# Optimization experiments

Measured on AMD Instinct MI355X. Metric: run time of the kernel, lower is better.

Reference implementation:

```python
import jax, jax.numpy as jnp
import numpy as np

N_NODES = 50000
N_EDGES = 800000
IN_C, HID_C, OUT_C = 100, 128, 40


def setup_inputs() -> dict:
    key = jax.random.key(0)
    ks = jax.random.split(key, 10)
    x = jax.random.normal(ks[0], (N_NODES, IN_C), dtype=jnp.float32)
    edge_index = jax.random.randint(ks[1], (2, N_EDGES), 0, N_NODES, dtype=jnp.int64)

    def lin(k, fan_in, fan_out):
        kw, kb = jax.random.split(k)
        bound = 1.0 / np.sqrt(fan_in)
        W = jax.random.uniform(kw, (fan_in, fan_out), minval=-bound, maxval=bound, dtype=jnp.float32)
        b = jax.random.uniform(kb, (fan_out,), minval=-bound, maxval=bound, dtype=jnp.float32)
        return W, b

    W1a, b1a = lin(ks[2], IN_C, HID_C)
    W1b, b1b = lin(ks[3], HID_C, HID_C)
    W2a, b2a = lin(ks[4], HID_C, OUT_C)
    W2b, b2b = lin(ks[5], OUT_C, OUT_C)
    return {"x": x, "edge_index": edge_index,
            "W1a": W1a, "b1a": b1a, "W1b": W1b, "b1b": b1b,
            "W2a": W2a, "b2a": b2a, "W2b": W2b, "b2b": b2b}


def _gin_aggregate(x, src, dst):
    # GINConv with eps=0: (1+eps)*x_i + sum_{j in N(i)} x_j
    msg_sum = jax.ops.segment_sum(x[src], dst, num_segments=N_NODES)
    return x + msg_sum


def reference(x, edge_index, W1a, b1a, W1b, b1b, W2a, b2a, W2b, b2b):
    src, dst = edge_index[0], edge_index[1]
    # ---- layer 1: GINConv(MLP[in, hid, hid]) + ReLU (dropout is identity in eval)
    h = _gin_aggregate(x, src, dst)                      # [N, in]
    h = jax.nn.relu(h @ W1a + b1a) @ W1b + b1b           # [N, hid]
    h = jax.nn.relu(h)
    # ---- layer 2: GINConv(MLP[hid, out, out]), no trailing act
    h = _gin_aggregate(h, src, dst)                      # [N, hid]
    logits = jax.nn.relu(h @ W2a + b2a) @ W2b + b2b      # [N, out]
    return jax.nn.log_softmax(logits, axis=1)
```

## Files before the change

kernel.cpp:

```cpp
#include <hip/hip_runtime.h>

#define NNODES 50000
#define INC 100
#define HIDC 128
#define OUTC 40
#define NB2 200
#define BSZ2 250
#define CAP2 6400
#define BIN_BLOCKS 256
#define EPB 13

typedef short bf16x8 __attribute__((ext_vector_type(8)));
typedef float f32x4 __attribute__((ext_vector_type(4)));

__device__ __forceinline__ unsigned short f2bf(float f) {
    unsigned int u = __float_as_uint(f);
    unsigned int r = (u + 0x7FFFu + ((u >> 16) & 1u)) >> 16;
    return (unsigned short)r;
}
__device__ __forceinline__ unsigned int pack2(float a, float b) {
    return (unsigned int)f2bf(a) | ((unsigned int)f2bf(b) << 16);
}
__device__ __forceinline__ float4 bf4(uint2 a) {
    return make_float4(__uint_as_float(a.x << 16), __uint_as_float(a.x & 0xFFFF0000u),
                       __uint_as_float(a.y << 16), __uint_as_float(a.y & 0xFFFF0000u));
}

__global__ __launch_bounds__(256) void prep_all(const float2* __restrict__ x2,
                                                unsigned int* __restrict__ xh, int n2,
                                                const float* __restrict__ W1a,
                                                unsigned short* __restrict__ Wt1a,
                                                const float* __restrict__ W1b,
                                                unsigned short* __restrict__ Wt1b,
                                                const float* __restrict__ W2a,
                                                unsigned short* __restrict__ Wt2a,
                                                const float* __restrict__ W2b,
                                                unsigned short* __restrict__ Wt2b,
                                                int* __restrict__ bcnt) {
    if (blockIdx.x == 0 && threadIdx.x < NB2) bcnt[threadIdx.x] = 0;
    int i = blockIdx.x * 256 + threadIdx.x;
    if (i < n2) {
        float2 v = x2[i];
        xh[i] = pack2(v.x, v.y);
        return;
    }
    i -= n2;
    if (i < 128 * 128) {
        int j = i >> 7, k = i & 127;
        Wt1a[i] = f2bf((k < INC) ? W1a[k * HIDC + j] : 0.f);
        return;
    }
    i -= 128 * 128;
    if (i < 128 * 128) {
        int j = i >> 7, k = i & 127;
        Wt1b[i] = f2bf(W1b[k * HIDC + j]);
        return;
    }
    i -= 128 * 128;
    if (i < 48 * 128) {
        int j = i >> 7, k = i & 127;
        Wt2a[i] = f2bf((j < OUTC) ? W2a[k * OUTC + j] : 0.f);
        return;
    }
    i -= 48 * 128;
    if (i < 48 * 64) {
        int j = i >> 6, k = i & 63;
        Wt2b[i] = f2bf((j < OUTC && k < OUTC) ? W2b[k * OUTC + j] : 0.f);
        return;
    }
}

__global__ __launch_bounds__(256) void bin_pairs(const int* __restrict__ src,
                                                 const int* __restrict__ dst,
                                                 int* __restrict__ bcnt,
                                                 unsigned int* __restrict__ pairs, int E) {
    __shared__ int bcount[NB2];
    __shared__ int bbase[NB2];
    __shared__ int bpos[NB2];
    int t = threadIdx.x;
    if (t < NB2) bcount[t] = 0;
    __syncthreads();
    int lo = (int)((long long)E * blockIdx.x / BIN_BLOCKS);
    int hi = (int)((long long)E * (blockIdx.x + 1) / BIN_BLOCKS);
    int myd[EPB];
#pragma unroll
    for (int k = 0; k < EPB; ++k) {
        int e = lo + t + k * 256;
        int d = (e < hi) ? dst[e] : -1;
        myd[k] = d;
        if (d >= 0) atomicAdd(&bcount[d / BSZ2], 1);
    }
    __syncthreads();
    if (t < NB2) {
        bbase[t] = atomicAdd(&bcnt[t], bcount[t]);
        bpos[t] = 0;
    }
    __syncthreads();
#pragma unroll
    for (int k = 0; k < EPB; ++k) {
        int d = myd[k];
        if (d >= 0) {
            int e = lo + t + k * 256;
            int s = src[e];
            int b = d / BSZ2;
            int rk = atomicAdd(&bpos[b], 1);
            pairs[(size_t)b * CAP2 + bbase[b] + rk] =
                ((unsigned int)d << 16) | (unsigned int)s;
        }
    }
}

__global__ __launch_bounds__(256) void build_bucket(const unsigned int* __restrict__ pairs,
                                                    const int* __restrict__ bcnt,
                                                    int* __restrict__ offs,
                                                    unsigned short* __restrict__ csr) {
    __shared__ int hist[BSZ2];
    __shared__ int cur[BSZ2];
    __shared__ int wsum[4];
    __shared__ int redbuf[4];
    __shared__ unsigned short lcsr[CAP2];
    __shared__ int base_s;

    const int b = blockIdx.x;
    const int t = threadIdx.x;
    const int lane = t & 63, wv = t >> 6;

    {
        int v = (t < b) ? bcnt[t] : 0;
#pragma unroll
        for (int off = 32; off; off >>= 1) v += __shfl_xor(v, off);
        if (lane == 0) redbuf[wv] = v;
    }
    if (t < BSZ2) hist[t] = 0;
    __syncthreads();
    if (t == 0) base_s = redbuf[0] + redbuf[1] + redbuf[2] + redbuf[3];

    const int cnt = bcnt[b];
    const unsigned int* P = pairs + (size_t)b * CAP2;
    const int nlo = b * BSZ2;
    __syncthreads();

    for (int i = t; i < cnt; i += 256)
        atomicAdd(&hist[(int)(P[i] >> 16) - nlo], 1);
    __syncthreads();

    {
        int v = (t < BSZ2) ? hist[t] : 0;
        int incl = v;
#pragma unroll
        for (int off = 1; off < 64; off <<= 1) {
            int u = __shfl_up(incl, off);
            if (lane >= off) incl += u;
        }
        if (lane == 63) wsum[wv] = incl;
        __syncthreads();
        int wbase = 0;
#pragma unroll
        for (int j = 0; j < 4; ++j)
            if (j < wv) wbase += wsum[j];
        int excl = wbase + incl - v;
        if (t < BSZ2) {
            cur[t] = excl;
            offs[nlo + t] = base_s + excl;
        }
        if (b == NB2 - 1 && t == 0) offs[NNODES] = base_s + cnt;
    }
    __syncthreads();

    for (int i = t; i < cnt; i += 256) {
        unsigned int pr = P[i];
        int pos = atomicAdd(&cur[(int)(pr >> 16) - nlo], 1);
        lcsr[pos] = (unsigned short)(pr & 0xFFFFu);
    }
    __syncthreads();

    for (int i = t; i < cnt; i += 256) csr[base_s + i] = lcsr[i];
}

__global__ __launch_bounds__(256) void agg_wide_bf(const float4* __restrict__ self,
                                                   const uint2* __restrict__ featbf,
                                                   const int* __restrict__ offs,
                                                   const unsigned short* __restrict__ csr,
                                                   unsigned short* __restrict__ Abf, int N) {
    constexpr int C4 = 25;
    int node = blockIdx.x * 8 + (threadIdx.x >> 5);
    int l = threadIdx.x & 31;
    if (node >= N) return;
    if (l >= C4) {
        *reinterpret_cast<uint2*>(&Abf[(size_t)node * 128 + l * 4]) = make_uint2(0u, 0u);
        return;
    }
    int s = offs[node], e = offs[node + 1];
    float4 acc = self[(size_t)node * C4 + l];
    int i = s;
    for (; i + 16 <= e; i += 16) {
        int n0 = (int)csr[i + 0],  n1 = (int)csr[i + 1];
        int n2 = (int)csr[i + 2],  n3 = (int)csr[i + 3];
        int n4 = (int)csr[i + 4],  n5 = (int)csr[i + 5];
        int n6 = (int)csr[i + 6],  n7 = (int)csr[i + 7];
        int n8 = (int)csr[i + 8],  n9 = (int)csr[i + 9];
        int na = (int)csr[i + 10], nb = (int)csr[i + 11];
        int nc = (int)csr[i + 12], nd = (int)csr[i + 13];
        int ne = (int)csr[i + 14], nf = (int)csr[i + 15];
        float4 v0 = bf4(featbf[(size_t)n0 * C4 + l]);
        float4 v1 = bf4(featbf[(size_t)n1 * C4 + l]);
        float4 v2 = bf4(featbf[(size_t)n2 * C4 + l]);
        float4 v3 = bf4(featbf[(size_t)n3 * C4 + l]);
        float4 v4 = bf4(featbf[(size_t)n4 * C4 + l]);
        float4 v5 = bf4(featbf[(size_t)n5 * C4 + l]);
        float4 v6 = bf4(featbf[(size_t)n6 * C4 + l]);
        float4 v7 = bf4(featbf[(size_t)n7 * C4 + l]);
        float4 v8 = bf4(featbf[(size_t)n8 * C4 + l]);
        float4 v9 = bf4(featbf[(size_t)n9 * C4 + l]);
        float4 va = bf4(featbf[(size_t)na * C4 + l]);
        float4 vb = bf4(featbf[(size_t)nb * C4 + l]);
        float4 vc = bf4(featbf[(size_t)nc * C4 + l]);
        float4 vd = bf4(featbf[(size_t)nd * C4 + l]);
        float4 ve = bf4(featbf[(size_t)ne * C4 + l]);
        float4 vf = bf4(featbf[(size_t)nf * C4 + l]);
        acc.x += (((v0.x + v1.x) + (v2.x + v3.x)) + ((v4.x + v5.x) + (v6.x + v7.x))) +
                 (((v8.x + v9.x) + (va.x + vb.x)) + ((vc.x + vd.x) + (ve.x + vf.x)));
        acc.y += (((v0.y + v1.y) + (v2.y + v3.y)) + ((v4.y + v5.y) + (v6.y + v7.y))) +
                 (((v8.y + v9.y) + (va.y + vb.y)) + ((vc.y + vd.y) + (ve.y + vf.y)));
        acc.z += (((v0.z + v1.z) + (v2.z + v3.z)) + ((v4.z + v5.z) + (v6.z + v7.z))) +
                 (((v8.z + v9.z) + (va.z + vb.z)) + ((vc.z + vd.z) + (ve.z + vf.z)));
        acc.w += (((v0.w + v1.w) + (v2.w + v3.w)) + ((v4.w + v5.w) + (v6.w + v7.w))) +
                 (((v8.w + v9.w) + (va.w + vb.w)) + ((vc.w + vd.w) + (ve.w + vf.w)));
    }
    for (; i + 8 <= e; i += 8) {
        int n0 = (int)csr[i + 0], n1 = (int)csr[i + 1];
        int n2 = (int)csr[i + 2], n3 = (int)csr[i + 3];
        int n4 = (int)csr[i + 4], n5 = (int)csr[i + 5];
        int n6 = (int)csr[i + 6], n7 = (int)csr[i + 7];
        float4 v0 = bf4(featbf[(size_t)n0 * C4 + l]);
        float4 v1 = bf4(featbf[(size_t)n1 * C4 + l]);
        float4 v2 = bf4(featbf[(size_t)n2 * C4 + l]);
        float4 v3 = bf4(featbf[(size_t)n3 * C4 + l]);
        float4 v4 = bf4(featbf[(size_t)n4 * C4 + l]);
        float4 v5 = bf4(featbf[(size_t)n5 * C4 + l]);
        float4 v6 = bf4(featbf[(size_t)n6 * C4 + l]);
        float4 v7 = bf4(featbf[(size_t)n7 * C4 + l]);
        acc.x += ((v0.x + v1.x) + (v2.x + v3.x)) + ((v4.x + v5.x) + (v6.x + v7.x));
        acc.y += ((v0.y + v1.y) + (v2.y + v3.y)) + ((v4.y + v5.y) + (v6.y + v7.y));
        acc.z += ((v0.z + v1.z) + (v2.z + v3.z)) + ((v4.z + v5.z) + (v6.z + v7.z));
        acc.w += ((v0.w + v1.w) + (v2.w + v3.w)) + ((v4.w + v5.w) + (v6.w + v7.w));
    }
    for (; i + 4 <= e; i += 4) {
        int n0 = (int)csr[i + 0], n1 = (int)csr[i + 1];
        int n2 = (int)csr[i + 2], n3 = (int)csr[i + 3];
        float4 v0 = bf4(featbf[(size_t)n0 * C4 + l]);
        float4 v1 = bf4(featbf[(size_t)n1 * C4 + l]);
        float4 v2 = bf4(featbf[(size_t)n2 * C4 + l]);
        float4 v3 = bf4(featbf[(size_t)n3 * C4 + l]);
        acc.x += (v0.x + v1.x) + (v2.x + v3.x);
        acc.y += (v0.y + v1.y) + (v2.y + v3.y);
        acc.z += (v0.z + v1.z) + (v2.z + v3.z);
        acc.w += (v0.w + v1.w) + (v2.w + v3.w);
    }
    for (; i < e; ++i) {
        int sn = (int)csr[i];
        float4 v = bf4(featbf[(size_t)sn * C4 + l]);
        acc.x += v.x; acc.y += v.y; acc.z += v.z; acc.w += v.w;
    }
    *reinterpret_cast<uint2*>(&Abf[(size_t)node * 128 + l * 4]) =
        make_uint2(pack2(acc.x, acc.y), pack2(acc.z, acc.w));
}

__global__ __launch_bounds__(256) void fused_mlp(const unsigned short* __restrict__ Abf,
                                                 const unsigned short* __restrict__ Wt1a,
                                                 const float* __restrict__ b1a,
                                                 const unsigned short* __restrict__ Wt1b,
                                                 const float* __restrict__ b1b,
                                                 const unsigned short* __restrict__ Wt2a,
                                                 unsigned short* __restrict__ Tb, int N) {
    constexpr int LDW = 136;
    __shared__ unsigned short As[64 * LDW];
    __shared__ unsigned short Ws[128 * LDW];
    __shared__ float bs1[128], bs2[128];

    const int tid = threadIdx.x;
    const int n0 = blockIdx.x * 64;

#pragma unroll
    for (int i = 0; i < 4; ++i) {
        int idx = tid + i * 256;
        int row = idx >> 4, c = idx & 15;
        int n = n0 + row;
        uint4 v = make_uint4(0u, 0u, 0u, 0u);
        if (n < N) v = *reinterpret_cast<const uint4*>(&Abf[(size_t)n * 128 + c * 8]);
        *reinterpret_cast<uint4*>(&As[row * LDW + c * 8]) = v;
    }
#pragma unroll
    for (int i = 0; i < 8; ++i) {
        int idx = tid + i * 256;
        int row = idx >> 4, c = idx & 15;
        *reinterpret_cast<uint4*>(&Ws[row * LDW + c * 8]) =
            *reinterpret_cast<const uint4*>(&Wt1a[(size_t)row * 128 + c * 8]);
    }
    if (tid < 128) { bs1[tid] = b1a[tid]; bs2[tid] = b1b[tid]; }
    __syncthreads();

    const int w = tid >> 6, l = tid & 63;
    const int wr = w >> 1, wc = w & 1;
    const int r = l & 15, g = l >> 4;

    f32x4 acc[2][4];
#pragma unroll
    for (int rt = 0; rt < 2; ++rt)
#pragma unroll
        for (int ct = 0; ct < 4; ++ct) {
            float b = bs1[wc * 64 + ct * 16 + r];
            acc[rt][ct] = (f32x4){b, b, b, b};
        }
#pragma unroll
    for (int s = 0; s < 4; ++s) {
        bf16x8 af[2], bfr[4];
#pragma unroll
        for (int rt = 0; rt < 2; ++rt)
            af[rt] = *reinterpret_cast<const bf16x8*>(
                &As[(wr * 32 + rt * 16 + r) * LDW + s * 32 + g * 8]);
#pragma unroll
        for (int ct = 0; ct < 4; ++ct)
            bfr[ct] = *reinterpret_cast<const bf16x8*>(
                &Ws[(wc * 64 + ct * 16 + r) * LDW + s * 32 + g * 8]);
#pragma unroll
        for (int rt = 0; rt < 2; ++rt)
#pragma unroll
            for (int ct = 0; ct < 4; ++ct)
                acc[rt][ct] = __builtin_amdgcn_mfma_f32_16x16x32_bf16(
                    af[rt], bfr[ct], acc[rt][ct], 0, 0, 0);
    }
    __syncthreads();

#pragma unroll
    for (int rt = 0; rt < 2; ++rt)
#pragma unroll
        for (int reg = 0; reg < 4; ++reg) {
            int row = wr * 32 + rt * 16 + 4 * g + reg;
#pragma unroll
            for (int ct = 0; ct < 4; ++ct) {
                int col = wc * 64 + ct * 16 + r;
                As[row * LDW + col] = f2bf(fmaxf(acc[rt][ct][reg], 0.f));
            }
        }
#pragma unroll
    for (int i = 0; i < 8; ++i) {
        int idx = tid + i * 256;
        int row = idx >> 4, c = idx & 15;
        *reinterpret_cast<uint4*>(&Ws[row * LDW + c * 8]) =
            *reinterpret_cast<const uint4*>(&Wt1b[(size_t)row * 128 + c * 8]);
    }
    __syncthreads();

#pragma unroll
    for (int rt = 0; rt < 2; ++rt)
#pragma unroll
        for (int ct = 0; ct < 4; ++ct) {
            float b = bs2[wc * 64 + ct * 16 + r];
            acc[rt][ct] = (f32x4){b, b, b, b};
        }
#pragma unroll
    for (int s = 0; s < 4; ++s) {
        bf16x8 af[2], bfr[4];
#pragma unroll
        for (int rt = 0; rt < 2; ++rt)
            af[rt] = *reinterpret_cast<const bf16x8*>(
                &As[(wr * 32 + rt * 16 + r) * LDW + s * 32 + g * 8]);
#pragma unroll
        for (int ct = 0; ct < 4; ++ct)
            bfr[ct] = *reinterpret_cast<const bf16x8*>(
                &Ws[(wc * 64 + ct * 16 + r) * LDW + s * 32 + g * 8]);
#pragma unroll
        for (int rt = 0; rt < 2; ++rt)
#pragma unroll
            for (int ct = 0; ct < 4; ++ct)
                acc[rt][ct] = __builtin_amdgcn_mfma_f32_16x16x32_bf16(
                    af[rt], bfr[ct], acc[rt][ct], 0, 0, 0);
    }
    __syncthreads();

#pragma unroll
    for (int rt = 0; rt < 2; ++rt)
#pragma unroll
        for (int reg = 0; reg < 4; ++reg) {
            int row = wr * 32 + rt * 16 + 4 * g + reg;
#pragma unroll
            for (int ct = 0; ct < 4; ++ct) {
                int col = wc * 64 + ct * 16 + r;
                As[row * LDW + col] = f2bf(fmaxf(acc[rt][ct][reg], 0.f));
            }
        }
#pragma unroll
    for (int i = 0; i < 3; ++i) {
        int idx = tid + i * 256;
        int row = idx >> 4, c = idx & 15;
        *reinterpret_cast<uint4*>(&Ws[row * LDW + c * 8]) =
            *reinterpret_cast<const uint4*>(&Wt2a[(size_t)row * 128 + c * 8]);
    }
    __syncthreads();

    f32x4 acc3[3] = {(f32x4){0, 0, 0, 0}, (f32x4){0, 0, 0, 0}, (f32x4){0, 0, 0, 0}};
#pragma unroll
    for (int s = 0; s < 4; ++s) {
        bf16x8 af = *reinterpret_cast<const bf16x8*>(
            &As[(w * 16 + r) * LDW + s * 32 + g * 8]);
#pragma unroll
        for (int ct = 0; ct < 3; ++ct) {
            bf16x8 bfr = *reinterpret_cast<const bf16x8*>(
                &Ws[(ct * 16 + r) * LDW + s * 32 + g * 8]);
            acc3[ct] = __builtin_amdgcn_mfma_f32_16x16x32_bf16(af, bfr, acc3[ct], 0, 0, 0);
        }
    }
#pragma unroll
    for (int reg = 0; reg < 4; ++reg) {
        int n = n0 + w * 16 + 4 * g + reg;
        if (n < N) {
#pragma unroll
            for (int ct = 0; ct < 3; ++ct) {
                int j = ct * 16 + r;
                if (j < OUTC) Tb[(size_t)n * OUTC + j] = f2bf(acc3[ct][reg]);
            }
        }
    }
}

__global__ __launch_bounds__(256) void agg40_bf(const uint2* __restrict__ Tbf,
                                                const int* __restrict__ offs,
                                                const unsigned short* __restrict__ csr,
                                                const float* __restrict__ b2a,
                                                unsigned short* __restrict__ Tb2, int N) {
    int wave = threadIdx.x >> 6;
    int lane = threadIdx.x & 63;
    int g = lane / 10;
    int sub = lane - g * 10;
    int node = blockIdx.x * 24 + wave * 6 + g;
    if (g >= 6 || node >= N) return;
    int s = offs[node], e = offs[node + 1];
    float4 acc = bf4(Tbf[(size_t)node * 10 + sub]);
    int i = s;
    for (; i + 8 <= e; i += 8) {
        int n0 = (int)csr[i + 0], n1 = (int)csr[i + 1];
        int n2 = (int)csr[i + 2], n3 = (int)csr[i + 3];
        int n4 = (int)csr[i + 4], n5 = (int)csr[i + 5];
        int n6 = (int)csr[i + 6], n7 = (int)csr[i + 7];
        float4 v0 = bf4(Tbf[(size_t)n0 * 10 + sub]);
        float4 v1 = bf4(Tbf[(size_t)n1 * 10 + sub]);
        float4 v2 = bf4(Tbf[(size_t)n2 * 10 + sub]);
        float4 v3 = bf4(Tbf[(size_t)n3 * 10 + sub]);
        float4 v4 = bf4(Tbf[(size_t)n4 * 10 + sub]);
        float4 v5 = bf4(Tbf[(size_t)n5 * 10 + sub]);
        float4 v6 = bf4(Tbf[(size_t)n6 * 10 + sub]);
        float4 v7 = bf4(Tbf[(size_t)n7 * 10 + sub]);
        acc.x += ((v0.x + v1.x) + (v2.x + v3.x)) + ((v4.x + v5.x) + (v6.x + v7.x));
        acc.y += ((v0.y + v1.y) + (v2.y + v3.y)) + ((v4.y + v5.y) + (v6.y + v7.y));
        acc.z += ((v0.z + v1.z) + (v2.z + v3.z)) + ((v4.z + v5.z) + (v6.z + v7.z));
        acc.w += ((v0.w + v1.w) + (v2.w + v3.w)) + ((v4.w + v5.w) + (v6.w + v7.w));
    }
    for (; i + 4 <= e; i += 4) {
        int n0 = (int)csr[i + 0], n1 = (int)csr[i + 1];
        int n2 = (int)csr[i + 2], n3 = (int)csr[i + 3];
        float4 v0 = bf4(Tbf[(size_t)n0 * 10 + sub]);
        float4 v1 = bf4(Tbf[(size_t)n1 * 10 + sub]);
        float4 v2 = bf4(Tbf[(size_t)n2 * 10 + sub]);
        float4 v3 = bf4(Tbf[(size_t)n3 * 10 + sub]);
        acc.x += (v0.x + v1.x) + (v2.x + v3.x);
        acc.y += (v0.y + v1.y) + (v2.y + v3.y);
        acc.z += (v0.z + v1.z) + (v2.z + v3.z);
        acc.w += (v0.w + v1.w) + (v2.w + v3.w);
    }
    for (; i < e; ++i) {
        int sn = (int)csr[i];
        float4 v = bf4(Tbf[(size_t)sn * 10 + sub]);
        acc.x += v.x; acc.y += v.y; acc.z += v.z; acc.w += v.w;
    }
    float4 ba = *reinterpret_cast<const float4*>(&b2a[sub * 4]);
    float t0 = fmaxf(acc.x + ba.x, 0.f);
    float t1 = fmaxf(acc.y + ba.y, 0.f);
    float t2 = fmaxf(acc.z + ba.z, 0.f);
    float t3 = fmaxf(acc.w + ba.w, 0.f);
    *reinterpret_cast<uint2*>(&Tb2[(size_t)node * 64 + sub * 4]) =
        make_uint2(pack2(t0, t1), pack2(t2, t3));
    if (sub < 6)
        *reinterpret_cast<uint2*>(&Tb2[(size_t)node * 64 + 40 + sub * 4]) =
            make_uint2(0u, 0u);
}

__global__ __launch_bounds__(256) void epi40_mfma(const unsigned short* __restrict__ Tb2,
                                                  const unsigned short* __restrict__ Wt2b,
                                                  const float* __restrict__ b2b,
                                                  float* __restrict__ out, int N) {
    constexpr int LDW = 72;
    __shared__ unsigned short As[64 * LDW];
    __shared__ unsigned short Ws[48 * LDW];
    __shared__ float bb[40];

    const int tid = threadIdx.x;
    const int n0 = blockIdx.x * 64;

    if (tid < 40) bb[tid] = b2b[tid];
    for (int idx = tid; idx < 384; idx += 256) {
        int row = idx >> 3, c = idx & 7;
        uint4 v = *reinterpret_cast<const uint4*>(&Wt2b[row * 64 + c * 8]);
        *reinterpret_cast<uint4*>(&Ws[row * LDW + c * 8]) = v;
    }
    for (int idx = tid; idx < 512; idx += 256) {
        int row = idx >> 3, c8 = idx & 7;
        int n = n0 + row;
        uint4 v = make_uint4(0u, 0u, 0u, 0u);
        if (n < N) v = *reinterpret_cast<const uint4*>(&Tb2[(size_t)n * 64 + c8 * 8]);
        *reinterpret_cast<uint4*>(&As[row * LDW + c8 * 8]) = v;
    }
    __syncthreads();

    const int w = tid >> 6, l = tid & 63;
    const int r = l & 15, g = l >> 4;

    f32x4 acc[3] = {(f32x4){0, 0, 0, 0}, (f32x4){0, 0, 0, 0}, (f32x4){0, 0, 0, 0}};
#pragma unroll
    for (int s = 0; s < 2; ++s) {
        bf16x8 af = *reinterpret_cast<const bf16x8*>(
            &As[(w * 16 + r) * LDW + s * 32 + g * 8]);
#pragma unroll
        for (int ct = 0; ct < 3; ++ct) {
            bf16x8 bfr = *reinterpret_cast<const bf16x8*>(
                &Ws[(ct * 16 + r) * LDW + s * 32 + g * 8]);
            acc[ct] = __builtin_amdgcn_mfma_f32_16x16x32_bf16(af, bfr, acc[ct], 0, 0, 0);
        }
    }

    float bb0 = bb[r], bb1 = bb[16 + r], bb2 = (r < 8) ? bb[32 + r] : 0.f;
#pragma unroll
    for (int reg = 0; reg < 4; ++reg) {
        int n = n0 + w * 16 + 4 * g + reg;
        float lg0 = acc[0][reg] + bb0;
        float lg1 = acc[1][reg] + bb1;
        float lg2 = (r < 8) ? acc[2][reg] + bb2 : -INFINITY;
        float m = fmaxf(fmaxf(lg0, lg1), lg2);
#pragma unroll
        for (int off = 1; off < 16; off <<= 1) m = fmaxf(m, __shfl_xor(m, off));
        float s = expf(lg0 - m) + expf(lg1 - m) + ((r < 8) ? expf(lg2 - m) : 0.f);
#pragma unroll
        for (int off = 1; off < 16; off <<= 1) s += __shfl_xor(s, off);
        float lse = m + logf(s);
        if (n < N) {
            out[(size_t)n * OUTC + r] = lg0 - lse;
            out[(size_t)n * OUTC + 16 + r] = lg1 - lse;
            if (r < 8) out[(size_t)n * OUTC + 32 + r] = lg2 - lse;
        }
    }
}

extern "C" void kernel_launch(void* const* d_in, const int* in_sizes, int n_in,
                              void* d_out, int out_size, void* d_ws, size_t ws_size,
                              hipStream_t stream) {
    const float* x   = (const float*)d_in[0];
    const int* edges = (const int*)d_in[1];
    const float* W1a = (const float*)d_in[2];
    const float* b1a = (const float*)d_in[3];
    const float* W1b = (const float*)d_in[4];
    const float* b1b = (const float*)d_in[5];
    const float* W2a = (const float*)d_in[6];
    const float* b2a = (const float*)d_in[7];
    const float* W2b = (const float*)d_in[8];
    const float* b2b = (const float*)d_in[9];

    const int N = NNODES;
    const int E = in_sizes[1] / 2;
    const int* srcp = edges;
    const int* dstp = edges + E;

    auto au = [](size_t v) { return (v + 255) & ~(size_t)255; };
    char* p = (char*)d_ws;
    int* bcnt    = (int*)p; p += au((size_t)NB2 * 4);
    int* offs    = (int*)p; p += au((size_t)(N + 1) * 4);
    unsigned int*   pairs = (unsigned int*)p;  p += au((size_t)NB2 * CAP2 * 4);
    unsigned short* csr   = (unsigned short*)p; p += au((size_t)E * 2);
    unsigned int*   xh   = (unsigned int*)p;   p += au((size_t)N * INC * 2);
    unsigned short* Abf  = (unsigned short*)p; p += au((size_t)N * 128 * 2);
    unsigned short* Tb   = (unsigned short*)p; p += au((size_t)N * OUTC * 2);
    unsigned short* Tb2  = (unsigned short*)p; p += au((size_t)N * 64 * 2);
    unsigned short* Wt1a = (unsigned short*)p; p += au((size_t)128 * 128 * 2);
    unsigned short* Wt1b = (unsigned short*)p; p += au((size_t)128 * 128 * 2);
    unsigned short* Wt2a = (unsigned short*)p; p += au((size_t)48 * 128 * 2);
    unsigned short* Wt2b = (unsigned short*)p; p += au((size_t)48 * 64 * 2);

    const int n2 = N * INC / 2;
    const int prep_total = n2 + 128 * 128 + 128 * 128 + 48 * 128 + 48 * 64;

    prep_all<<<(prep_total + 255) / 256, 256, 0, stream>>>(
        (const float2*)x, xh, n2, W1a, Wt1a, W1b, Wt1b, W2a, Wt2a, W2b, Wt2b, bcnt);

    bin_pairs<<<BIN_BLOCKS, 256, 0, stream>>>(srcp, dstp, bcnt, pairs, E);
    build_bucket<<<NB2, 256, 0, stream>>>(pairs, bcnt, offs, csr);

    agg_wide_bf<<<(N + 7) / 8, 256, 0, stream>>>((const float4*)x, (const uint2*)xh,
                                                 offs, csr, Abf, N);
    fused_mlp<<<(N + 63) / 64, 256, 0, stream>>>(Abf, Wt1a, b1a, Wt1b, b1b, Wt2a, Tb, N);

    agg40_bf<<<(N + 23) / 24, 256, 0, stream>>>((const uint2*)Tb, offs, csr, b2a, Tb2, N);
    epi40_mfma<<<(N + 63) / 64, 256, 0, stream>>>(Tb2, Wt2b, b2b, (float*)d_out, N);
}
```

Measured before the change: 103.8 us.

## Merge prep with edge binning and fuse layer-2 aggregation into MFMA epilogue

```diff
diff --git a/kernel.cpp b/kernel.cpp
--- a/kernel.cpp
+++ b/kernel.cpp
@@ -26,19 +26,60 @@
                        __uint_as_float(a.y << 16), __uint_as_float(a.y & 0xFFFF0000u));
 }
 
-__global__ __launch_bounds__(256) void prep_all(const float2* __restrict__ x2,
-                                                unsigned int* __restrict__ xh, int n2,
-                                                const float* __restrict__ W1a,
-                                                unsigned short* __restrict__ Wt1a,
-                                                const float* __restrict__ W1b,
-                                                unsigned short* __restrict__ Wt1b,
-                                                const float* __restrict__ W2a,
-                                                unsigned short* __restrict__ Wt2a,
-                                                const float* __restrict__ W2b,
-                                                unsigned short* __restrict__ Wt2b,
-                                                int* __restrict__ bcnt) {
-    if (blockIdx.x == 0 && threadIdx.x < NB2) bcnt[threadIdx.x] = 0;
-    int i = blockIdx.x * 256 + threadIdx.x;
+__global__ __launch_bounds__(256) void stage1(const int* __restrict__ src,
+                                              const int* __restrict__ dst,
+                                              int* __restrict__ bcnt,
+                                              unsigned int* __restrict__ pairs, int E,
+                                              const float2* __restrict__ x2,
+                                              unsigned int* __restrict__ xh, int n2,
+                                              const float* __restrict__ W1a,
+                                              unsigned short* __restrict__ Wt1a,
+                                              const float* __restrict__ W1b,
+                                              unsigned short* __restrict__ Wt1b,
+                                              const float* __restrict__ W2a,
+                                              unsigned short* __restrict__ Wt2a,
+                                              const float* __restrict__ W2b,
+                                              unsigned short* __restrict__ Wt2b) {
+    __shared__ int bcount[NB2];
+    __shared__ int bbase[NB2];
+    __shared__ int bpos[NB2];
+    const int t = threadIdx.x;
+
+    if (blockIdx.x < BIN_BLOCKS) {
+        if (t < NB2) bcount[t] = 0;
+        __syncthreads();
+        int lo = (int)((long long)E * blockIdx.x / BIN_BLOCKS);
+        int hi = (int)((long long)E * (blockIdx.x + 1) / BIN_BLOCKS);
+        int myd[EPB];
+#pragma unroll
+        for (int k = 0; k < EPB; ++k) {
+            int e = lo + t + k * 256;
+            int d = (e < hi) ? dst[e] : -1;
+            myd[k] = d;
+            if (d >= 0) atomicAdd(&bcount[d / BSZ2], 1);
+        }
+        __syncthreads();
+        if (t < NB2) {
+            bbase[t] = atomicAdd(&bcnt[t], bcount[t]);
+            bpos[t] = 0;
+        }
+        __syncthreads();
+#pragma unroll
+        for (int k = 0; k < EPB; ++k) {
+            int d = myd[k];
+            if (d >= 0) {
+                int e = lo + t + k * 256;
+                int s = src[e];
+                int b = d / BSZ2;
+                int rk = atomicAdd(&bpos[b], 1);
+                pairs[(size_t)b * CAP2 + bbase[b] + rk] =
+                    ((unsigned int)d << 16) | (unsigned int)s;
+            }
+        }
+        return;
+    }
+
+    int i = (blockIdx.x - BIN_BLOCKS) * 256 + t;
     if (i < n2) {
         float2 v = x2[i];
         xh[i] = pack2(v.x, v.y);
@@ -67,46 +108,6 @@
         int j = i >> 6, k = i & 63;
         Wt2b[i] = f2bf((j < OUTC && k < OUTC) ? W2b[k * OUTC + j] : 0.f);
         return;
-    }
-}
-
-__global__ __launch_bounds__(256) void bin_pairs(const int* __restrict__ src,
-                                                 const int* __restrict__ dst,
-                                                 int* __restrict__ bcnt,
-                                                 unsigned int* __restrict__ pairs, int E) {
-    __shared__ int bcount[NB2];
-    __shared__ int bbase[NB2];
-    __shared__ int bpos[NB2];
-    int t = threadIdx.x;
-    if (t < NB2) bcount[t] = 0;
-    __syncthreads();
-    int lo = (int)((long long)E * blockIdx.x / BIN_BLOCKS);
-    int hi = (int)((long long)E * (blockIdx.x + 1) / BIN_BLOCKS);
-    int myd[EPB];
-#pragma unroll
-    for (int k = 0; k < EPB; ++k) {
-        int e = lo + t + k * 256;
-        int d = (e < hi) ? dst[e] : -1;
-        myd[k] = d;
-        if (d >= 0) atomicAdd(&bcount[d / BSZ2], 1);
-    }
-    __syncthreads();
-    if (t < NB2) {
-        bbase[t] = atomicAdd(&bcnt[t], bcount[t]);
-        bpos[t] = 0;
-    }
-    __syncthreads();
-#pragma unroll
-    for (int k = 0; k < EPB; ++k) {
-        int d = myd[k];
-        if (d >= 0) {
-            int e = lo + t + k * 256;
-            int s = src[e];
-            int b = d / BSZ2;
-            int rk = atomicAdd(&bpos[b], 1);
-            pairs[(size_t)b * CAP2 + bbase[b] + rk] =
-                ((unsigned int)d << 16) | (unsigned int)s;
-        }
     }
 }
 
@@ -424,71 +425,13 @@
     }
 }
 
-__global__ __launch_bounds__(256) void agg40_bf(const uint2* __restrict__ Tbf,
-                                                const int* __restrict__ offs,
-                                                const unsigned short* __restrict__ csr,
-                                                const float* __restrict__ b2a,
-                                                unsigned short* __restrict__ Tb2, int N) {
-    int wave = threadIdx.x >> 6;
-    int lane = threadIdx.x & 63;
-    int g = lane / 10;
-    int sub = lane - g * 10;
-    int node = blockIdx.x * 24 + wave * 6 + g;
-    if (g >= 6 || node >= N) return;
-    int s = offs[node], e = offs[node + 1];
-    float4 acc = bf4(Tbf[(size_t)node * 10 + sub]);
-    int i = s;
-    for (; i + 8 <= e; i += 8) {
-        int n0 = (int)csr[i + 0], n1 = (int)csr[i + 1];
-        int n2 = (int)csr[i + 2], n3 = (int)csr[i + 3];
-        int n4 = (int)csr[i + 4], n5 = (int)csr[i + 5];
-        int n6 = (int)csr[i + 6], n7 = (int)csr[i + 7];
-        float4 v0 = bf4(Tbf[(size_t)n0 * 10 + sub]);
-        float4 v1 = bf4(Tbf[(size_t)n1 * 10 + sub]);
-        float4 v2 = bf4(Tbf[(size_t)n2 * 10 + sub]);
-        float4 v3 = bf4(Tbf[(size_t)n3 * 10 + sub]);
-        float4 v4 = bf4(Tbf[(size_t)n4 * 10 + sub]);
-        float4 v5 = bf4(Tbf[(size_t)n5 * 10 + sub]);
-        float4 v6 = bf4(Tbf[(size_t)n6 * 10 + sub]);
-        float4 v7 = bf4(Tbf[(size_t)n7 * 10 + sub]);
-        acc.x += ((v0.x + v1.x) + (v2.x + v3.x)) + ((v4.x + v5.x) + (v6.x + v7.x));
-        acc.y += ((v0.y + v1.y) + (v2.y + v3.y)) + ((v4.y + v5.y) + (v6.y + v7.y));
-        acc.z += ((v0.z + v1.z) + (v2.z + v3.z)) + ((v4.z + v5.z) + (v6.z + v7.z));
-        acc.w += ((v0.w + v1.w) + (v2.w + v3.w)) + ((v4.w + v5.w) + (v6.w + v7.w));
-    }
-    for (; i + 4 <= e; i += 4) {
-        int n0 = (int)csr[i + 0], n1 = (int)csr[i + 1];
-        int n2 = (int)csr[i + 2], n3 = (int)csr[i + 3];
-        float4 v0 = bf4(Tbf[(size_t)n0 * 10 + sub]);
-        float4 v1 = bf4(Tbf[(size_t)n1 * 10 + sub]);
-        float4 v2 = bf4(Tbf[(size_t)n2 * 10 + sub]);
-        float4 v3 = bf4(Tbf[(size_t)n3 * 10 + sub]);
-        acc.x += (v0.x + v1.x) + (v2.x + v3.x);
-        acc.y += (v0.y + v1.y) + (v2.y + v3.y);
-        acc.z += (v0.z + v1.z) + (v2.z + v3.z);
-        acc.w += (v0.w + v1.w) + (v2.w + v3.w);
-    }
-    for (; i < e; ++i) {
-        int sn = (int)csr[i];
-        float4 v = bf4(Tbf[(size_t)sn * 10 + sub]);
-        acc.x += v.x; acc.y += v.y; acc.z += v.z; acc.w += v.w;
-    }
-    float4 ba = *reinterpret_cast<const float4*>(&b2a[sub * 4]);
-    float t0 = fmaxf(acc.x + ba.x, 0.f);
-    float t1 = fmaxf(acc.y + ba.y, 0.f);
-    float t2 = fmaxf(acc.z + ba.z, 0.f);
-    float t3 = fmaxf(acc.w + ba.w, 0.f);
-    *reinterpret_cast<uint2*>(&Tb2[(size_t)node * 64 + sub * 4]) =
-        make_uint2(pack2(t0, t1), pack2(t2, t3));
-    if (sub < 6)
-        *reinterpret_cast<uint2*>(&Tb2[(size_t)node * 64 + 40 + sub * 4]) =
-            make_uint2(0u, 0u);
-}
-
-__global__ __launch_bounds__(256) void epi40_mfma(const unsigned short* __restrict__ Tb2,
-                                                  const unsigned short* __restrict__ Wt2b,
-                                                  const float* __restrict__ b2b,
-                                                  float* __restrict__ out, int N) {
+__global__ __launch_bounds__(256) void agg_epi40(const uint2* __restrict__ Tbf,
+                                                 const int* __restrict__ offs,
+                                                 const unsigned short* __restrict__ csr,
+                                                 const float* __restrict__ b2a,
+                                                 const unsigned short* __restrict__ Wt2b,
+                                                 const float* __restrict__ b2b,
+                                                 float* __restrict__ out, int N) {
     constexpr int LDW = 72;
     __shared__ unsigned short As[64 * LDW];
     __shared__ unsigned short Ws[48 * LDW];
@@ -503,12 +446,63 @@
         uint4 v = *reinterpret_cast<const uint4*>(&Wt2b[row * 64 + c * 8]);
         *reinterpret_cast<uint4*>(&Ws[row * LDW + c * 8]) = v;
     }
-    for (int idx = tid; idx < 512; idx += 256) {
-        int row = idx >> 3, c8 = idx & 7;
-        int n = n0 + row;
-        uint4 v = make_uint4(0u, 0u, 0u, 0u);
-        if (n < N) v = *reinterpret_cast<const uint4*>(&Tb2[(size_t)n * 64 + c8 * 8]);
-        *reinterpret_cast<uint4*>(&As[row * LDW + c8 * 8]) = v;
+    for (int idx = tid; idx < 64 * 6; idx += 256) {
+        int row = idx / 6, c = idx - row * 6;
+        *reinterpret_cast<uint2*>(&As[row * LDW + 40 + c * 4]) = make_uint2(0u, 0u);
+    }
+
+    for (int rep = 0; rep < 3; ++rep) {
+        int task = rep * 256 + tid;
+        if (task >= 640) break;
+        int nl = task / 10;
+        int sub = task - nl * 10;
+        int node = n0 + nl;
+        if (node >= N) continue;
+        int s = offs[node], e = offs[node + 1];
+        float4 acc = bf4(Tbf[(size_t)node * 10 + sub]);
+        int i = s;
+        for (; i + 8 <= e; i += 8) {
+            int m0 = (int)csr[i + 0], m1 = (int)csr[i + 1];
+            int m2 = (int)csr[i + 2], m3 = (int)csr[i + 3];
+            int m4 = (int)csr[i + 4], m5 = (int)csr[i + 5];
+            int m6 = (int)csr[i + 6], m7 = (int)csr[i + 7];
+            float4 v0 = bf4(Tbf[(size_t)m0 * 10 + sub]);
+            float4 v1 = bf4(Tbf[(size_t)m1 * 10 + sub]);
+            float4 v2 = bf4(Tbf[(size_t)m2 * 10 + sub]);
+            float4 v3 = bf4(Tbf[(size_t)m3 * 10 + sub]);
+            float4 v4 = bf4(Tbf[(size_t)m4 * 10 + sub]);
+            float4 v5 = bf4(Tbf[(size_t)m5 * 10 + sub]);
+            float4 v6 = bf4(Tbf[(size_t)m6 * 10 + sub]);
+            float4 v7 = bf4(Tbf[(size_t)m7 * 10 + sub]);
+            acc.x += ((v0.x + v1.x) + (v2.x + v3.x)) + ((v4.x + v5.x) + (v6.x + v7.x));
+            acc.y += ((v0.y + v1.y) + (v2.y + v3.y)) + ((v4.y + v5.y) + (v6.y + v7.y));
+            acc.z += ((v0.z + v1.z) + (v2.z + v3.z)) + ((v4.z + v5.z) + (v6.z + v7.z));
+            acc.w += ((v0.w + v1.w) + (v2.w + v3.w)) + ((v4.w + v5.w) + (v6.w + v7.w));
+        }
+        for (; i + 4 <= e; i += 4) {
+            int m0 = (int)csr[i + 0], m1 = (int)csr[i + 1];
+            int m2 = (int)csr[i + 2], m3 = (int)csr[i + 3];
+            float4 v0 = bf4(Tbf[(size_t)m0 * 10 + sub]);
+            float4 v1 = bf4(Tbf[(size_t)m1 * 10 + sub]);
+            float4 v2 = bf4(Tbf[(size_t)m2 * 10 + sub]);
+            float4 v3 = bf4(Tbf[(size_t)m3 * 10 + sub]);
+            acc.x += (v0.x + v1.x) + (v2.x + v3.x);
+            acc.y += (v0.y + v1.y) + (v2.y + v3.y);
+            acc.z += (v0.z + v1.z) + (v2.z + v3.z);
+            acc.w += (v0.w + v1.w) + (v2.w + v3.w);
+        }
+        for (; i < e; ++i) {
+            int sn = (int)csr[i];
+            float4 v = bf4(Tbf[(size_t)sn * 10 + sub]);
+            acc.x += v.x; acc.y += v.y; acc.z += v.z; acc.w += v.w;
+        }
+        float4 ba = *reinterpret_cast<const float4*>(&b2a[sub * 4]);
+        float t0 = fmaxf(acc.x + ba.x, 0.f);
+        float t1 = fmaxf(acc.y + ba.y, 0.f);
+        float t2 = fmaxf(acc.z + ba.z, 0.f);
+        float t3 = fmaxf(acc.w + ba.w, 0.f);
+        *reinterpret_cast<uint2*>(&As[nl * LDW + sub * 4]) =
+            make_uint2(pack2(t0, t1), pack2(t2, t3));
     }
     __syncthreads();
 
@@ -578,7 +572,6 @@
     unsigned int*   xh   = (unsigned int*)p;   p += au((size_t)N * INC * 2);
     unsigned short* Abf  = (unsigned short*)p; p += au((size_t)N * 128 * 2);
     unsigned short* Tb   = (unsigned short*)p; p += au((size_t)N * OUTC * 2);
-    unsigned short* Tb2  = (unsigned short*)p; p += au((size_t)N * 64 * 2);
     unsigned short* Wt1a = (unsigned short*)p; p += au((size_t)128 * 128 * 2);
     unsigned short* Wt1b = (unsigned short*)p; p += au((size_t)128 * 128 * 2);
     unsigned short* Wt2a = (unsigned short*)p; p += au((size_t)48 * 128 * 2);
@@ -586,17 +579,19 @@
 
     const int n2 = N * INC / 2;
     const int prep_total = n2 + 128 * 128 + 128 * 128 + 48 * 128 + 48 * 64;
-
-    prep_all<<<(prep_total + 255) / 256, 256, 0, stream>>>(
-        (const float2*)x, xh, n2, W1a, Wt1a, W1b, Wt1b, W2a, Wt2a, W2b, Wt2b, bcnt);
-
-    bin_pairs<<<BIN_BLOCKS, 256, 0, stream>>>(srcp, dstp, bcnt, pairs, E);
+    const int prep_blocks = (prep_total + 255) / 256;
+
+    hipMemsetAsync(bcnt, 0, (size_t)NB2 * sizeof(int), stream);
+    stage1<<<BIN_BLOCKS + prep_blocks, 256, 0, stream>>>(
+        srcp, dstp, bcnt, pairs, E,
+        (const float2*)x, xh, n2, W1a, Wt1a, W1b, Wt1b, W2a, Wt2a, W2b, Wt2b);
+
     build_bucket<<<NB2, 256, 0, stream>>>(pairs, bcnt, offs, csr);
 
     agg_wide_bf<<<(N + 7) / 8, 256, 0, stream>>>((const float4*)x, (const uint2*)xh,
                                                  offs, csr, Abf, N);
     fused_mlp<<<(N + 63) / 64, 256, 0, stream>>>(Abf, Wt1a, b1a, Wt1b, b1b, Wt2a, Tb, N);
 
-    agg40_bf<<<(N + 23) / 24, 256, 0, stream>>>((const uint2*)Tb, offs, csr, b2a, Tb2, N);
-    epi40_mfma<<<(N + 63) / 64, 256, 0, stream>>>(Tb2, Wt2b, b2b, (float*)d_out, N);
-}
+    agg_epi40<<<(N + 63) / 64, 256, 0, stream>>>((const uint2*)Tb, offs, csr, b2a,
+                                                 Wt2b, b2b, (float*)d_out, N);
+}
```

After: 104.0 us. No clear change (+0.2%).
